# Kernel tuning notes

Hardware: AMD Instinct MI355X
Metric: run time of the kernel (lower is better)

Reference implementation:

```python
import jax, jax.numpy as jnp
import numpy as np

N_NODES = 20000
N_EDGES = 320000
IN_DIM = 256
HIDDEN = 256
OUT_DIM = 128
N_LAYERS = 3
N_GROUPS = 4
EXP_PER_GROUP = 2
N_EXPERTS = N_GROUPS * EXP_PER_GROUP
TOP_K = 2


def setup_inputs() -> dict:
    key = jax.random.key(0)
    ks = jax.random.split(key, 12)
    d = HIDDEN
    r = 2 * d  # router/expert input dim: concat(node, neighbor-mean)
    x = jax.random.normal(ks[0], (N_NODES, IN_DIM), dtype=jnp.float32)
    edge_index = jax.random.randint(ks[1], (2, N_EDGES), 0, N_NODES, dtype=jnp.int32)
    s = 0.05
    Wg = jax.random.normal(ks[2], (N_LAYERS, r, N_GROUPS), dtype=jnp.float32) * s
    We = jax.random.normal(ks[3], (N_LAYERS, r, N_EXPERTS), dtype=jnp.float32) * s
    Ww = jax.random.normal(ks[4], (N_LAYERS, r, d), dtype=jnp.float32) * s
    W1 = jax.random.normal(ks[5], (N_LAYERS, N_EXPERTS, r, d), dtype=jnp.float32) * s
    b1 = jnp.zeros((N_LAYERS, N_EXPERTS, d), dtype=jnp.float32)
    W2 = jax.random.normal(ks[6], (N_LAYERS, N_EXPERTS, d, d), dtype=jnp.float32) * s
    b2 = jnp.zeros((N_LAYERS, N_EXPERTS, d), dtype=jnp.float32)
    wc = jax.random.normal(ks[7], (N_LAYERS, r, 1), dtype=jnp.float32) * s
    Wout = jax.random.normal(ks[8], (d, OUT_DIM), dtype=jnp.float32) * s
    return {"x": x, "edge_index": edge_index, "Wg": Wg, "We": We, "Ww": Ww,
            "W1": W1, "b1": b1, "W2": W2, "b2": b2, "wc": wc, "Wout": Wout}


def _moe_layer(h, src, dst, deg, Wg, We, Ww, W1, b1, W2, b2, wc):
    N = h.shape[0]
    # graph message passing: mean aggregation over incoming edges
    agg = jax.ops.segment_sum(h[src], dst, num_segments=N) / deg  # [N, d]
    r = jnp.concatenate([h, agg], axis=-1)  # [N, 2d] combined router input
    # hierarchical routing: group softmax x within-group expert softmax
    gp = jax.nn.softmax(r @ Wg, axis=-1)                                # [N, G]
    ep = jax.nn.softmax((r @ We).reshape(N, N_GROUPS, EXP_PER_GROUP), axis=-1)
    probs = (gp[..., None] * ep).reshape(N, N_EXPERTS)                  # [N, E]
    # top-k gating, renormalized
    topv, topi = jax.lax.top_k(probs, TOP_K)
    gates = jnp.zeros_like(probs).at[jnp.arange(N)[:, None], topi].set(topv)
    gates = gates / (gates.sum(-1, keepdims=True) + 1e-9)              # [N, E]
    # strong experts: per-expert 2-layer MLP, combined by gates
    hid = jax.nn.relu(jnp.einsum('nf,efd->ned', r, W1) + b1[None])      # [N, E, d]
    exp_out = jnp.einsum('ned,edo->neo', hid, W2) + b2[None]            # [N, E, d]
    strong = jnp.einsum('ne,neo->no', gates, exp_out)                   # [N, d]
    # weak shared expert + confidence gate blend
    weak = r @ Ww                                                       # [N, d]
    conf = jax.nn.sigmoid(r @ wc)                                       # [N, 1]
    return jax.nn.relu(conf * strong + (1.0 - conf) * weak)


def reference(x, edge_index, Wg, We, Ww, W1, b1, W2, b2, wc, Wout):
    src, dst = edge_index[0], edge_index[1]
    N = x.shape[0]
    deg = jax.ops.segment_sum(jnp.ones((edge_index.shape[1],), jnp.float32), dst,
                              num_segments=N)
    deg = jnp.maximum(deg, 1.0)[:, None]
    h = x
    for l in range(Wg.shape[0]):  # small fixed layer loop
        h = _moe_layer(h, src, dst, deg, Wg[l], We[l], Ww[l],
                       W1[l], b1[l], W2[l], b2[l], wc[l])
    return h @ Wout
```

## Files before the change

### kernel.cpp

```cpp
#include <hip/hip_runtime.h>

#define NN 20000
#define NEDGE 320000
#define D 256
#define RD 512
#define OD 128
#define NEXP 8
#define NSLOT (2*NN)
#define NODE_BLOCKS 79
#define ASSIGN_BLOCKS 157

typedef unsigned short u16;
typedef __attribute__((ext_vector_type(8))) short short8v;
typedef __attribute__((ext_vector_type(16))) float f32x16;

__device__ __forceinline__ void split1(float v, u16& h, u16& m, u16& l) {
    unsigned b = __float_as_uint(v);
    h = (u16)(b >> 16);
    float fh = __uint_as_float(b & 0xffff0000u);
    float r1 = v - fh;
    unsigned b1 = __float_as_uint(r1);
    m = (u16)(b1 >> 16);
    float fm = __uint_as_float(b1 & 0xffff0000u);
    float r2 = r1 - fm;
    l = (u16)(__float_as_uint(r2) >> 16);
}

__device__ __forceinline__ void split8(const float4& x, const float4& y,
                                       short8v& h, short8v& m, short8v& l) {
    float v[8] = {x.x, x.y, x.z, x.w, y.x, y.y, y.z, y.w};
#pragma unroll
    for (int i = 0; i < 8; i++) {
        u16 hh, mm, ll;
        split1(v[i], hh, mm, ll);
        h[i] = (short)hh; m[i] = (short)mm; l[i] = (short)ll;
    }
}


__global__ void copy_x_zero_cnt_k(const float* __restrict__ x, float* __restrict__ r,
                                  int* __restrict__ cnt) {
    int gid = blockIdx.x * 256 + threadIdx.x;
    int n = gid >> 6;
    int c4 = gid & 63;
    if (gid < NN * (D / 4)) {
        float4 v = reinterpret_cast<const float4*>(x)[gid];
        reinterpret_cast<float4*>(r + (size_t)n * RD)[c4] = v;
    }
    if (gid < NN) cnt[gid] = 0;
}

__global__ void count_edges_k(const int* __restrict__ dst, int* __restrict__ cnt) {
    int e = blockIdx.x * 256 + threadIdx.x;
    if (e < NEDGE) atomicAdd(&cnt[dst[e]], 1);
}

__global__ void block_sums_k(const int* __restrict__ cnt, int* __restrict__ bsum) {
    __shared__ int s[256];
    int i = blockIdx.x * 256 + threadIdx.x;
    s[threadIdx.x] = (i < NN) ? cnt[i] : 0;
    __syncthreads();
    for (int off = 128; off > 0; off >>= 1) {
        if (threadIdx.x < off) s[threadIdx.x] += s[threadIdx.x + off];
        __syncthreads();
    }
    if (threadIdx.x == 0) bsum[blockIdx.x] = s[0];
}

__global__ void scan_bsums_k(int* __restrict__ bsum, int* __restrict__ row_start) {
    if (blockIdx.x == 0 && threadIdx.x == 0) {
        int acc = 0;
        for (int i = 0; i < NODE_BLOCKS; i++) { int t = bsum[i]; bsum[i] = acc; acc += t; }
        row_start[NN] = acc;
    }
}

__global__ void block_scan_k(const int* __restrict__ cnt, const int* __restrict__ bsum,
                             int* __restrict__ row_start, int* __restrict__ cur) {
    __shared__ int s[256];
    int i = blockIdx.x * 256 + threadIdx.x;
    int v = (i < NN) ? cnt[i] : 0;
    s[threadIdx.x] = v;
    __syncthreads();
    for (int off = 1; off < 256; off <<= 1) {
        int t = (threadIdx.x >= off) ? s[threadIdx.x - off] : 0;
        __syncthreads();
        s[threadIdx.x] += t;
        __syncthreads();
    }
    int excl = s[threadIdx.x] - v + bsum[blockIdx.x];
    if (i < NN) { row_start[i] = excl; cur[i] = excl; }
}

__global__ void fill_csr_k(const int* __restrict__ src, const int* __restrict__ dst,
                           int* __restrict__ cur, int* __restrict__ csr_src) {
    int e = blockIdx.x * 256 + threadIdx.x;
    if (e < NEDGE) {
        int pos = atomicAdd(&cur[dst[e]], 1);
        csr_src[pos] = src[e];
    }
}

__global__ void aggregate_k(float* __restrict__ r, const int* __restrict__ row_start,
                            const int* __restrict__ csr_src, int* __restrict__ ec) {
    if (blockIdx.x == 0 && threadIdx.x < 16) ec[threadIdx.x] = 0;
    int wid = blockIdx.x * 4 + (threadIdx.x >> 6);
    int lane = threadIdx.x & 63;
    if (wid >= NN) return;
    int beg = row_start[wid], end = row_start[wid + 1];
    float ax = 0.f, ay = 0.f, az = 0.f, aw = 0.f;
    for (int j = beg; j < end; j++) {
        int s = csr_src[j];
        float4 v = reinterpret_cast<const float4*>(r + (size_t)s * RD)[lane];
        ax += v.x; ay += v.y; az += v.z; aw += v.w;
    }
    float deg = (float)((end - beg) > 1 ? (end - beg) : 1);
    float4 o = make_float4(ax / deg, ay / deg, az / deg, aw / deg);
    reinterpret_cast<float4*>(r + (size_t)wid * RD + D)[lane] = o;
}

__global__ void router_k(const float* __restrict__ r, const float* __restrict__ Wg,
                         const float* __restrict__ We, const float* __restrict__ wc,
                         int* __restrict__ node_top, float* __restrict__ node_gate,
                         float* __restrict__ conf) {
    int wid = blockIdx.x * 4 + (threadIdx.x >> 6);
    int lane = threadIdx.x & 63;
    if (wid >= NN) return;

    const float* rrow = r + (size_t)wid * RD;
    float pg[4] = {0, 0, 0, 0};
    float pe[8] = {0, 0, 0, 0, 0, 0, 0, 0};
    float pc = 0.f;
#pragma unroll
    for (int i = 0; i < 8; i++) {
        int k = lane + i * 64;
        float rv = rrow[k];
        float4 wg = *reinterpret_cast<const float4*>(Wg + (size_t)k * 4);
        pg[0] = fmaf(rv, wg.x, pg[0]); pg[1] = fmaf(rv, wg.y, pg[1]);
        pg[2] = fmaf(rv, wg.z, pg[2]); pg[3] = fmaf(rv, wg.w, pg[3]);
        float4 w0 = *reinterpret_cast<const float4*>(We + (size_t)k * 8);
        float4 w1 = *reinterpret_cast<const float4*>(We + (size_t)k * 8 + 4);
        pe[0] = fmaf(rv, w0.x, pe[0]); pe[1] = fmaf(rv, w0.y, pe[1]);
        pe[2] = fmaf(rv, w0.z, pe[2]); pe[3] = fmaf(rv, w0.w, pe[3]);
        pe[4] = fmaf(rv, w1.x, pe[4]); pe[5] = fmaf(rv, w1.y, pe[5]);
        pe[6] = fmaf(rv, w1.z, pe[6]); pe[7] = fmaf(rv, w1.w, pe[7]);
        pc = fmaf(rv, wc[k], pc);
    }
#pragma unroll
    for (int off = 32; off > 0; off >>= 1) {
#pragma unroll
        for (int g = 0; g < 4; g++) pg[g] += __shfl_xor(pg[g], off);
#pragma unroll
        for (int g = 0; g < 8; g++) pe[g] += __shfl_xor(pe[g], off);
        pc += __shfl_xor(pc, off);
    }

    if (lane == 0) {
        float m = fmaxf(fmaxf(pg[0], pg[1]), fmaxf(pg[2], pg[3]));
        float eg[4]; float sg = 0.f;
#pragma unroll
        for (int g = 0; g < 4; g++) { eg[g] = expf(pg[g] - m); sg += eg[g]; }
        float probs[8];
#pragma unroll
        for (int g = 0; g < 4; g++) {
            float a = pe[2 * g], b = pe[2 * g + 1];
            float mm = fmaxf(a, b);
            float ea = expf(a - mm), eb = expf(b - mm);
            float inv = 1.f / (ea + eb);
            float gp = eg[g] / sg;
            probs[2 * g]     = gp * ea * inv;
            probs[2 * g + 1] = gp * eb * inv;
        }
        int i0 = 0; float v0 = probs[0];
#pragma unroll
        for (int j = 1; j < 8; j++) if (probs[j] > v0) { v0 = probs[j]; i0 = j; }
        int i1 = -1; float v1 = -1e30f;
#pragma unroll
        for (int j = 0; j < 8; j++) if (j != i0 && probs[j] > v1) { v1 = probs[j]; i1 = j; }
        float s = v0 + v1 + 1e-9f;
        node_top[2 * wid] = i0;  node_top[2 * wid + 1] = i1;
        node_gate[2 * wid] = v0 / s;  node_gate[2 * wid + 1] = v1 / s;
        conf[wid] = 1.f / (1.f + expf(-pc));
    }
}

__global__ void expert_hist_k(const int* __restrict__ node_top, int* __restrict__ ec) {
    __shared__ int h[NEXP];
    if (threadIdx.x < NEXP) h[threadIdx.x] = 0;
    __syncthreads();
    int i = blockIdx.x * 256 + threadIdx.x;
    if (i < NSLOT) atomicAdd(&h[node_top[i]], 1);
    __syncthreads();
    if (threadIdx.x < NEXP && h[threadIdx.x] > 0) atomicAdd(&ec[threadIdx.x], h[threadIdx.x]);
}

__global__ void expert_scan_k(const int* __restrict__ ec, int* __restrict__ es,
                              int* __restrict__ ecur) {
    if (blockIdx.x == 0 && threadIdx.x == 0) {
        int acc = 0;
        for (int e = 0; e < NEXP; e++) { es[e] = acc; acc += ec[e]; ecur[e] = 0; }
        es[NEXP] = acc;
    }
}

__global__ void fill_experts_k(const int* __restrict__ node_top, const float* __restrict__ node_gate,
                               const int* __restrict__ es, int* __restrict__ ecur,
                               int* __restrict__ slot_node, float* __restrict__ slot_gate,
                               int* __restrict__ node_slot) {
    __shared__ int hcnt[NEXP], hbase[NEXP];
    int tid = threadIdx.x;
    if (tid < NEXP) hcnt[tid] = 0;
    __syncthreads();
    int i = blockIdx.x * 256 + tid;
    int e = 0, local = 0;
    bool act = (i < NSLOT);
    if (act) {
        e = node_top[i];
        local = atomicAdd(&hcnt[e], 1);
    }
    __syncthreads();
    if (tid < NEXP) hbase[tid] = (hcnt[tid] > 0) ? atomicAdd(&ecur[tid], hcnt[tid]) : 0;
    __syncthreads();
    if (act) {
        int slot = es[e] + hbase[e] + local;
        slot_node[slot] = i >> 1;
        slot_gate[slot] = node_gate[i];
        node_slot[i] = slot;
    }
}

__global__ void combine_k(const float* __restrict__ expout, const float* __restrict__ weak,
                          const float* __restrict__ conf, const int* __restrict__ node_slot,
                          float* __restrict__ r) {
    int gid = blockIdx.x * 256 + threadIdx.x;
    if (gid >= NN * (D / 4)) return;
    int n = gid >> 6, c4 = gid & 63;
    int s0 = node_slot[2 * n], s1 = node_slot[2 * n + 1];
    float4 e0 = reinterpret_cast<const float4*>(expout + (size_t)s0 * D)[c4];
    float4 e1 = reinterpret_cast<const float4*>(expout + (size_t)s1 * D)[c4];
    float4 w  = reinterpret_cast<const float4*>(weak + (size_t)n * D)[c4];
    float cf = conf[n], cg = 1.f - cf;
    float4 o;
    o.x = fmaxf(cf * (e0.x + e1.x) + cg * w.x, 0.f);
    o.y = fmaxf(cf * (e0.y + e1.y) + cg * w.y, 0.f);
    o.z = fmaxf(cf * (e0.z + e1.z) + cg * w.z, 0.f);
    o.w = fmaxf(cf * (e0.w + e1.w) + cg * w.w, 0.f);
    reinterpret_cast<float4*>(r + (size_t)n * RD)[c4] = o;
}

__global__ void btile_k(const float* __restrict__ src, u16* __restrict__ dH,
                        u16* __restrict__ dM, u16* __restrict__ dL,
                        int K, int N, int total) {
    int gid = blockIdx.x * 256 + threadIdx.x;
    if (gid >= total) return;
    int l = gid & 63;
    int tile = gid >> 6;
    int K16 = K >> 4;
    int kb = tile % K16;
    int t2 = tile / K16;
    int N32 = N >> 5;
    int nb = t2 % N32;
    int mat = t2 / N32;
    int kbase = (kb << 4) + ((l >> 5) << 3);
    int n = (nb << 5) + (l & 31);
    const float* s = src + ((size_t)mat * K + kbase) * N + n;
    short8v vh, vm, vl;
#pragma unroll
    for (int j = 0; j < 8; j++) {
        u16 hh, mm, ll;
        split1(s[(size_t)j * N], hh, mm, ll);
        vh[j] = (short)hh; vm[j] = (short)mm; vl[j] = (short)ll;
    }
    size_t o = (size_t)gid * 8;
    *reinterpret_cast<short8v*>(dH + o) = vh;
    *reinterpret_cast<short8v*>(dM + o) = vm;
    *reinterpret_cast<short8v*>(dL + o) = vl;
}

template <int MODE>
__global__ __launch_bounds__(256, 3) void gemm_mfma(
    const float* __restrict__ A, int lda,
    const u16* __restrict__ BH, const u16* __restrict__ BM,
    const u16* __restrict__ BL,
    const float* __restrict__ bias,
    float* __restrict__ C, int ldc,
    const int* __restrict__ es,
    const int* __restrict__ slot_node,
    const float* __restrict__ slot_gate,
    int M, int N, int K) {
    constexpr int LDK2 = 24;
    constexpr int PL2 = 128 * LDK2;
    __shared__ u16 sA[3 * PL2];

    int tid = threadIdx.x;
    int row0, valid_rows;
    if (MODE == 0) {
        row0 = blockIdx.x * 128;
        valid_rows = M - row0; if (valid_rows > 128) valid_rows = 128;
    } else {
        int bx = blockIdx.x, acc0 = 0, expert = -1, mt = 0;
        row0 = 0; valid_rows = 0;
        for (int e = 0; e < NEXP; e++) {
            int c = es[e + 1] - es[e];
            int t = (c + 127) >> 7;
            if (bx < acc0 + t) {
                expert = e; mt = bx - acc0; row0 = es[e] + (mt << 7);
                valid_rows = c - (mt << 7); if (valid_rows > 128) valid_rows = 128;
                break;
            }
            acc0 += t;
        }
        if (expert < 0) return;
        size_t bo = (size_t)expert * N * K;
        BH += bo; BM += bo; BL += bo;
        bias += expert * D;
    }
    int ncol0 = blockIdx.y * 128;

    int srow = tid >> 1;
    int koff = (tid & 1) * 8;
    int grow;
    {
        int i0 = row0 + srow;
        if (MODE == 1) {
            i0 = i0 < NSLOT ? i0 : NSLOT - 1;
            grow = slot_node[i0];
        } else {
            grow = i0 < M ? i0 : M - 1;
        }
    }
    const float* pA = A + (size_t)grow * lda + koff;

    int lane = tid & 63;
    int wr = ((tid >> 7) & 1) * 64;
    int wc = ((tid >> 6) & 1) * 64;
    int fl = lane & 31;
    int fh8 = (lane >> 5) * 8;
    int K16 = K >> 4;
    int nb0 = (ncol0 + wc) >> 5;
    size_t tb0 = ((size_t)nb0 * K16) * 512 + (size_t)lane * 8;
    size_t tb1 = ((size_t)(nb0 + 1) * K16) * 512 + (size_t)lane * 8;

    f32x16 acc[2][2] = {};
    int aoff = srow * LDK2 + koff;
    const u16* Af0 = sA + (wr + fl) * LDK2 + fh8;
    const u16* Af1 = Af0 + 32 * LDK2;

    for (int kt = 0; kt < K; kt += 16) {
        float4 av0 = *reinterpret_cast<const float4*>(pA + kt);
        float4 av1 = *reinterpret_cast<const float4*>(pA + kt + 4);
        size_t o0 = tb0 + (size_t)(kt >> 4) * 512;
        size_t o1 = tb1 + (size_t)(kt >> 4) * 512;
        short8v bH0 = *reinterpret_cast<const short8v*>(BH + o0);
        short8v bM0 = *reinterpret_cast<const short8v*>(BM + o0);
        short8v bL0 = *reinterpret_cast<const short8v*>(BL + o0);
        short8v bH1 = *reinterpret_cast<const short8v*>(BH + o1);
        short8v bM1 = *reinterpret_cast<const short8v*>(BM + o1);
        short8v bL1 = *reinterpret_cast<const short8v*>(BL + o1);
        __syncthreads();
        {
            short8v h, m, l;
            split8(av0, av1, h, m, l);
            *reinterpret_cast<short8v*>(&sA[0 * PL2 + aoff]) = h;
            *reinterpret_cast<short8v*>(&sA[1 * PL2 + aoff]) = m;
            *reinterpret_cast<short8v*>(&sA[2 * PL2 + aoff]) = l;
        }
        __syncthreads();
        short8v aH0 = *reinterpret_cast<const short8v*>(Af0);
        short8v aM0 = *reinterpret_cast<const short8v*>(Af0 + PL2);
        short8v aL0 = *reinterpret_cast<const short8v*>(Af0 + 2 * PL2);
        short8v aH1 = *reinterpret_cast<const short8v*>(Af1);
        short8v aM1 = *reinterpret_cast<const short8v*>(Af1 + PL2);
        short8v aL1 = *reinterpret_cast<const short8v*>(Af1 + 2 * PL2);
#define MFMA_ACC(d, a, b) d = __builtin_amdgcn_mfma_f32_32x32x16_bf16(a, b, d, 0, 0, 0)
        MFMA_ACC(acc[0][0], aH0, bH0); MFMA_ACC(acc[0][0], aH0, bM0);
        MFMA_ACC(acc[0][0], aM0, bH0); MFMA_ACC(acc[0][0], aH0, bL0);
        MFMA_ACC(acc[0][0], aM0, bM0); MFMA_ACC(acc[0][0], aL0, bH0);
        MFMA_ACC(acc[0][1], aH0, bH1); MFMA_ACC(acc[0][1], aH0, bM1);
        MFMA_ACC(acc[0][1], aM0, bH1); MFMA_ACC(acc[0][1], aH0, bL1);
        MFMA_ACC(acc[0][1], aM0, bM1); MFMA_ACC(acc[0][1], aL0, bH1);
        MFMA_ACC(acc[1][0], aH1, bH0); MFMA_ACC(acc[1][0], aH1, bM0);
        MFMA_ACC(acc[1][0], aM1, bH0); MFMA_ACC(acc[1][0], aH1, bL0);
        MFMA_ACC(acc[1][0], aM1, bM0); MFMA_ACC(acc[1][0], aL1, bH0);
        MFMA_ACC(acc[1][1], aH1, bH1); MFMA_ACC(acc[1][1], aH1, bM1);
        MFMA_ACC(acc[1][1], aM1, bH1); MFMA_ACC(acc[1][1], aH1, bL1);
        MFMA_ACC(acc[1][1], aM1, bM1); MFMA_ACC(acc[1][1], aL1, bH1);
#undef MFMA_ACC
    }

    int fh = lane >> 5;
#pragma unroll
    for (int i = 0; i < 2; i++) {
#pragma unroll
        for (int j = 0; j < 2; j++) {
            int colg = ncol0 + wc + j * 32 + fl;
            float bv = (MODE != 0) ? bias[colg] : 0.f;
#pragma unroll
            for (int rg = 0; rg < 16; rg++) {
                int lrow = wr + i * 32 + (rg & 3) + 8 * (rg >> 2) + 4 * fh;
                if (lrow >= valid_rows) continue;
                int growo = row0 + lrow;
                float v = acc[i][j][rg] + bv;
                if (MODE == 1) {
                    v = fmaxf(v, 0.f);
                } else if (MODE == 2) {
                    v *= slot_gate[growo];
                }
                C[(size_t)growo * ldc + colg] = v;
            }
        }
    }
}

extern "C" void kernel_launch(void* const* d_in, const int* in_sizes, int n_in,
                              void* d_out, int out_size, void* d_ws, size_t ws_size,
                              hipStream_t stream) {
    (void)in_sizes; (void)n_in; (void)out_size; (void)ws_size;
    const float* x    = (const float*)d_in[0];
    const int*   ei   = (const int*)d_in[1];
    const float* Wg   = (const float*)d_in[2];
    const float* We   = (const float*)d_in[3];
    const float* Ww   = (const float*)d_in[4];
    const float* W1   = (const float*)d_in[5];
    const float* b1   = (const float*)d_in[6];
    const float* W2   = (const float*)d_in[7];
    const float* b2   = (const float*)d_in[8];
    const float* wcp  = (const float*)d_in[9];
    const float* Wout = (const float*)d_in[10];
    float* out = (float*)d_out;

    char* p = (char*)d_ws;
    auto alloc = [&](size_t bytes) -> char* {
        char* q = p; p += (bytes + 255) & ~(size_t)255; return q;
    };
    int*   cnt       = (int*)alloc((size_t)NN * 4);
    int*   row_start = (int*)alloc((size_t)(NN + 1) * 4);
    int*   cur       = (int*)alloc((size_t)NN * 4);
    int*   bsum      = (int*)alloc(128 * 4);
    int*   csr_src   = (int*)alloc((size_t)NEDGE * 4);
    float* r         = (float*)alloc((size_t)NN * RD * 4);
    float* hid       = (float*)alloc((size_t)NSLOT * D * 4);
    float* expout    = (float*)alloc((size_t)NSLOT * D * 4);
    float* conf      = (float*)alloc((size_t)NN * 4);
    int*   node_top  = (int*)alloc((size_t)2 * NN * 4);
    float* node_gate = (float*)alloc((size_t)2 * NN * 4);
    int*   node_slot = (int*)alloc((size_t)2 * NN * 4);
    int*   slot_node = (int*)alloc((size_t)NSLOT * 4);
    float* slot_gate = (float*)alloc((size_t)NSLOT * 4);
    int*   ec        = (int*)alloc(64 * 4);
    int*   es        = (int*)alloc(64 * 4);
    int*   ecur      = (int*)alloc(64 * 4);
    u16* w1tH = (u16*)alloc((size_t)NEXP * D * RD * 2);
    u16* w1tM = (u16*)alloc((size_t)NEXP * D * RD * 2);
    u16* w1tL = (u16*)alloc((size_t)NEXP * D * RD * 2);
    u16* w2tH = (u16*)alloc((size_t)NEXP * D * D * 2);
    u16* w2tM = (u16*)alloc((size_t)NEXP * D * D * 2);
    u16* w2tL = (u16*)alloc((size_t)NEXP * D * D * 2);
    u16* wwtH = (u16*)alloc((size_t)D * RD * 2);
    u16* wwtM = (u16*)alloc((size_t)D * RD * 2);
    u16* wwtL = (u16*)alloc((size_t)D * RD * 2);
    u16* wotH = (u16*)alloc((size_t)OD * D * 2);
    u16* wotM = (u16*)alloc((size_t)OD * D * 2);
    u16* wotL = (u16*)alloc((size_t)OD * D * 2);
    float* weak = hid;

    const int* srcp = ei;
    const int* dstp = ei + NEDGE;
    const int EB = (NEDGE + 255) / 256;

    copy_x_zero_cnt_k<<<5000, 256, 0, stream>>>(x, r, cnt);
    count_edges_k<<<EB, 256, 0, stream>>>(dstp, cnt);
    block_sums_k<<<NODE_BLOCKS, 256, 0, stream>>>(cnt, bsum);
    scan_bsums_k<<<1, 64, 0, stream>>>(bsum, row_start);
    block_scan_k<<<NODE_BLOCKS, 256, 0, stream>>>(cnt, bsum, row_start, cur);
    fill_csr_k<<<EB, 256, 0, stream>>>(srcp, dstp, cur, csr_src);
    btile_k<<<16, 256, 0, stream>>>(Wout, wotH, wotM, wotL, D, OD, 4096);

    for (int l = 0; l < 3; l++) {
        btile_k<<<512, 256, 0, stream>>>(W1 + (size_t)l * NEXP * RD * D,
                                         w1tH, w1tM, w1tL, RD, D, 131072);
        btile_k<<<256, 256, 0, stream>>>(W2 + (size_t)l * NEXP * D * D,
                                         w2tH, w2tM, w2tL, D, D, 65536);
        btile_k<<<64, 256, 0, stream>>>(Ww + (size_t)l * RD * D,
                                        wwtH, wwtM, wwtL, RD, D, 16384);
        aggregate_k<<<5000, 256, 0, stream>>>(r, row_start, csr_src, ec);
        router_k<<<5000, 256, 0, stream>>>(r,
            Wg + (size_t)l * RD * 4, We + (size_t)l * RD * 8, wcp + (size_t)l * RD,
            node_top, node_gate, conf);
        expert_hist_k<<<ASSIGN_BLOCKS, 256, 0, stream>>>(node_top, ec);
        expert_scan_k<<<1, 64, 0, stream>>>(ec, es, ecur);
        fill_experts_k<<<ASSIGN_BLOCKS, 256, 0, stream>>>(node_top, node_gate, es, ecur,
                                                          slot_node, slot_gate, node_slot);
        gemm_mfma<1><<<dim3(320, 2), 256, 0, stream>>>(r, RD, w1tH, w1tM, w1tL,
            b1 + (size_t)l * NEXP * D, hid, D, es, slot_node, slot_gate, NSLOT, D, RD);
        gemm_mfma<2><<<dim3(320, 2), 256, 0, stream>>>(hid, D, w2tH, w2tM, w2tL,
            b2 + (size_t)l * NEXP * D, expout, D, es, slot_node, slot_gate, NSLOT, D, D);
        gemm_mfma<0><<<dim3(157, 2), 256, 0, stream>>>(r, RD, wwtH, wwtM, wwtL,
            nullptr, weak, D, nullptr, nullptr, nullptr, NN, D, RD);
        combine_k<<<5000, 256, 0, stream>>>(expout, weak, conf, node_slot, r);
    }
    gemm_mfma<0><<<dim3(157, 1), 256, 0, stream>>>(r, RD, wotH, wotM, wotL,
        nullptr, out, OD, nullptr, nullptr, nullptr, NN, OD, D);
}
```

Before: 840.8 us.

## Double-buffer A tile in LDS and prefetch next K-slice in GEMM

Reworks the MFMA GEMM main loop to ping-pong between two LDS buffers holding the split bf16 A tile. The next K-slice's global loads are issued before computing the current one, which halves the barriers per 16-wide K step and overlaps load latency with MFMA work. In exchange LDS use doubles and launch bounds drop from 3 to 2 blocks per CU, which can lower occupancy and latency hiding. It also assumes K is a multiple of 32.

Measured after the change: 873.7 us. 1.04x slower.

```diff
diff --git a/kernel.cpp b/kernel.cpp
--- a/kernel.cpp
+++ b/kernel.cpp
@@ -278,7 +278,7 @@
 }
 
 template <int MODE>
-__global__ __launch_bounds__(256, 3) void gemm_mfma(
+__global__ __launch_bounds__(256, 2) void gemm_mfma(
     const float* __restrict__ A, int lda,
     const u16* __restrict__ BH, const u16* __restrict__ BM,
     const u16* __restrict__ BL,
@@ -290,7 +290,7 @@
     int M, int N, int K) {
     constexpr int LDK2 = 24;
     constexpr int PL2 = 128 * LDK2;
-    __shared__ u16 sA[3 * PL2];
+    __shared__ u16 sA[6 * PL2];
 
     int tid = threadIdx.x;
     int row0, valid_rows;
@@ -343,35 +343,24 @@
 
     f32x16 acc[2][2] = {};
     int aoff = srow * LDK2 + koff;
-    const u16* Af0 = sA + (wr + fl) * LDK2 + fh8;
-    const u16* Af1 = Af0 + 32 * LDK2;
-
-    for (int kt = 0; kt < K; kt += 16) {
-        float4 av0 = *reinterpret_cast<const float4*>(pA + kt);
-        float4 av1 = *reinterpret_cast<const float4*>(pA + kt + 4);
-        size_t o0 = tb0 + (size_t)(kt >> 4) * 512;
-        size_t o1 = tb1 + (size_t)(kt >> 4) * 512;
-        short8v bH0 = *reinterpret_cast<const short8v*>(BH + o0);
-        short8v bM0 = *reinterpret_cast<const short8v*>(BM + o0);
-        short8v bL0 = *reinterpret_cast<const short8v*>(BL + o0);
-        short8v bH1 = *reinterpret_cast<const short8v*>(BH + o1);
-        short8v bM1 = *reinterpret_cast<const short8v*>(BM + o1);
-        short8v bL1 = *reinterpret_cast<const short8v*>(BL + o1);
-        __syncthreads();
-        {
-            short8v h, m, l;
-            split8(av0, av1, h, m, l);
-            *reinterpret_cast<short8v*>(&sA[0 * PL2 + aoff]) = h;
-            *reinterpret_cast<short8v*>(&sA[1 * PL2 + aoff]) = m;
-            *reinterpret_cast<short8v*>(&sA[2 * PL2 + aoff]) = l;
-        }
-        __syncthreads();
-        short8v aH0 = *reinterpret_cast<const short8v*>(Af0);
-        short8v aM0 = *reinterpret_cast<const short8v*>(Af0 + PL2);
-        short8v aL0 = *reinterpret_cast<const short8v*>(Af0 + 2 * PL2);
-        short8v aH1 = *reinterpret_cast<const short8v*>(Af1);
-        short8v aM1 = *reinterpret_cast<const short8v*>(Af1 + PL2);
-        short8v aL1 = *reinterpret_cast<const short8v*>(Af1 + 2 * PL2);
+
+    auto stage = [&](u16* buf, const float4& x, const float4& y) {
+        short8v h, m, l;
+        split8(x, y, h, m, l);
+        *reinterpret_cast<short8v*>(buf + 0 * PL2 + aoff) = h;
+        *reinterpret_cast<short8v*>(buf + 1 * PL2 + aoff) = m;
+        *reinterpret_cast<short8v*>(buf + 2 * PL2 + aoff) = l;
+    };
+    auto do_tile = [&](const u16* buf, short8v bH0, short8v bM0, short8v bL0,
+                       short8v bH1, short8v bM1, short8v bL1) {
+        const u16* A0 = buf + (wr + fl) * LDK2 + fh8;
+        const u16* A1 = A0 + 32 * LDK2;
+        short8v aH0 = *reinterpret_cast<const short8v*>(A0);
+        short8v aM0 = *reinterpret_cast<const short8v*>(A0 + PL2);
+        short8v aL0 = *reinterpret_cast<const short8v*>(A0 + 2 * PL2);
+        short8v aH1 = *reinterpret_cast<const short8v*>(A1);
+        short8v aM1 = *reinterpret_cast<const short8v*>(A1 + PL2);
+        short8v aL1 = *reinterpret_cast<const short8v*>(A1 + 2 * PL2);
 #define MFMA_ACC(d, a, b) d = __builtin_amdgcn_mfma_f32_32x32x16_bf16(a, b, d, 0, 0, 0)
         MFMA_ACC(acc[0][0], aH0, bH0); MFMA_ACC(acc[0][0], aH0, bM0);
         MFMA_ACC(acc[0][0], aM0, bH0); MFMA_ACC(acc[0][0], aH0, bL0);
@@ -386,6 +375,51 @@
         MFMA_ACC(acc[1][1], aM1, bH1); MFMA_ACC(acc[1][1], aH1, bL1);
         MFMA_ACC(acc[1][1], aM1, bM1); MFMA_ACC(acc[1][1], aL1, bH1);
 #undef MFMA_ACC
+    };
+
+    float4 av0 = *reinterpret_cast<const float4*>(pA);
+    float4 av1 = *reinterpret_cast<const float4*>(pA + 4);
+    short8v cH0 = *reinterpret_cast<const short8v*>(BH + tb0);
+    short8v cM0 = *reinterpret_cast<const short8v*>(BM + tb0);
+    short8v cL0 = *reinterpret_cast<const short8v*>(BL + tb0);
+    short8v cH1 = *reinterpret_cast<const short8v*>(BH + tb1);
+    short8v cM1 = *reinterpret_cast<const short8v*>(BM + tb1);
+    short8v cL1 = *reinterpret_cast<const short8v*>(BL + tb1);
+    stage(sA, av0, av1);
+    __syncthreads();
+
+    for (int kt = 0; kt < K; kt += 32) {
+        float4 nv0 = *reinterpret_cast<const float4*>(pA + kt + 16);
+        float4 nv1 = *reinterpret_cast<const float4*>(pA + kt + 20);
+        size_t o0 = tb0 + (size_t)((kt >> 4) + 1) * 512;
+        size_t o1 = tb1 + (size_t)((kt >> 4) + 1) * 512;
+        short8v nH0 = *reinterpret_cast<const short8v*>(BH + o0);
+        short8v nM0 = *reinterpret_cast<const short8v*>(BM + o0);
+        short8v nL0 = *reinterpret_cast<const short8v*>(BL + o0);
+        short8v nH1 = *reinterpret_cast<const short8v*>(BH + o1);
+        short8v nM1 = *reinterpret_cast<const short8v*>(BM + o1);
+        short8v nL1 = *reinterpret_cast<const short8v*>(BL + o1);
+        do_tile(sA, cH0, cM0, cL0, cH1, cM1, cL1);
+        stage(sA + 3 * PL2, nv0, nv1);
+        __syncthreads();
+        bool more = (kt + 32 < K);
+        if (more) {
+            av0 = *reinterpret_cast<const float4*>(pA + kt + 32);
+            av1 = *reinterpret_cast<const float4*>(pA + kt + 36);
+            o0 = tb0 + (size_t)((kt >> 4) + 2) * 512;
+            o1 = tb1 + (size_t)((kt >> 4) + 2) * 512;
+            cH0 = *reinterpret_cast<const short8v*>(BH + o0);
+            cM0 = *reinterpret_cast<const short8v*>(BM + o0);
+            cL0 = *reinterpret_cast<const short8v*>(BL + o0);
+            cH1 = *reinterpret_cast<const short8v*>(BH + o1);
+            cM1 = *reinterpret_cast<const short8v*>(BM + o1);
+            cL1 = *reinterpret_cast<const short8v*>(BL + o1);
+        }
+        do_tile(sA + 3 * PL2, nH0, nM0, nL0, nH1, nM1, nL1);
+        if (more) {
+            stage(sA, av0, av1);
+        }
+        __syncthreads();
     }
 
     int fh = lane >> 5;
```

## Halve GEMM row tile to 64 with swizzled fragment LDS layout

Applied to the files above, without the earlier changes.

The 3-way bf16-split MFMA GEMM's row tile shrinks from 128 to 64. Each wave now computes 32x64 instead of 64x64, and the grids double, so more blocks are resident and the tail is smaller. The A tile is stored in LDS in an MFMA-fragment-ordered layout without padding, and launch bounds rise to 5 blocks/CU. The cost is that each B fragment is reused across half as many rows, which roughly doubles B-tile global traffic per output and lowers MFMA work per barrier.

Measured after the change: 825.3 us. Within noise of the previous version (-1.9%).

```diff
diff --git a/kernel.cpp b/kernel.cpp
--- a/kernel.cpp
+++ b/kernel.cpp
@@ -11,6 +11,7 @@
 #define ASSIGN_BLOCKS 157
 
 typedef unsigned short u16;
+typedef __attribute__((ext_vector_type(4))) short short4v;
 typedef __attribute__((ext_vector_type(8))) short short8v;
 typedef __attribute__((ext_vector_type(16))) float f32x16;
 
@@ -24,17 +25,6 @@
     float fm = __uint_as_float(b1 & 0xffff0000u);
     float r2 = r1 - fm;
     l = (u16)(__float_as_uint(r2) >> 16);
-}
-
-__device__ __forceinline__ void split8(const float4& x, const float4& y,
-                                       short8v& h, short8v& m, short8v& l) {
-    float v[8] = {x.x, x.y, x.z, x.w, y.x, y.y, y.z, y.w};
-#pragma unroll
-    for (int i = 0; i < 8; i++) {
-        u16 hh, mm, ll;
-        split1(v[i], hh, mm, ll);
-        h[i] = (short)hh; m[i] = (short)mm; l[i] = (short)ll;
-    }
 }
 
 
@@ -278,7 +268,7 @@
 }
 
 template <int MODE>
-__global__ __launch_bounds__(256, 3) void gemm_mfma(
+__global__ __launch_bounds__(256, 5) void gemm_mfma(
     const float* __restrict__ A, int lda,
     const u16* __restrict__ BH, const u16* __restrict__ BM,
     const u16* __restrict__ BL,
@@ -288,37 +278,36 @@
     const int* __restrict__ slot_node,
     const float* __restrict__ slot_gate,
     int M, int N, int K) {
-    constexpr int LDK2 = 24;
-    constexpr int PL2 = 128 * LDK2;
+    constexpr int PL2 = 1024;
     __shared__ u16 sA[3 * PL2];
 
     int tid = threadIdx.x;
     int row0, valid_rows;
     if (MODE == 0) {
-        row0 = blockIdx.x * 128;
-        valid_rows = M - row0; if (valid_rows > 128) valid_rows = 128;
+        row0 = blockIdx.x * 64;
+        valid_rows = M - row0; if (valid_rows > 64) valid_rows = 64;
     } else {
         int bx = blockIdx.x, acc0 = 0, expert = -1, mt = 0;
         row0 = 0; valid_rows = 0;
         for (int e = 0; e < NEXP; e++) {
             int c = es[e + 1] - es[e];
-            int t = (c + 127) >> 7;
+            int t = (c + 63) >> 6;
             if (bx < acc0 + t) {
-                expert = e; mt = bx - acc0; row0 = es[e] + (mt << 7);
-                valid_rows = c - (mt << 7); if (valid_rows > 128) valid_rows = 128;
+                expert = e; mt = bx - acc0; row0 = es[e] + (mt << 6);
+                valid_rows = c - (mt << 6); if (valid_rows > 64) valid_rows = 64;
                 break;
             }
             acc0 += t;
         }
         if (expert < 0) return;
-        size_t bo = (size_t)expert * N * K;
+        int bo = expert * N * K;
         BH += bo; BM += bo; BL += bo;
         bias += expert * D;
     }
     int ncol0 = blockIdx.y * 128;
 
-    int srow = tid >> 1;
-    int koff = (tid & 1) * 8;
+    int srow = tid >> 2;
+    int koff = (tid & 3) * 4;
     int grow;
     {
         int i0 = row0 + srow;
@@ -330,84 +319,77 @@
         }
     }
     const float* pA = A + (size_t)grow * lda + koff;
+    int woff = ((srow >> 5) * 2 + (koff >> 3)) * 256 + (srow & 31) * 8 + (koff & 4);
 
     int lane = tid & 63;
-    int wr = ((tid >> 7) & 1) * 64;
-    int wc = ((tid >> 6) & 1) * 64;
+    int wave = tid >> 6;
+    int wr = (wave & 1) * 32;
+    int wc = (wave >> 1) * 64;
     int fl = lane & 31;
-    int fh8 = (lane >> 5) * 8;
     int K16 = K >> 4;
     int nb0 = (ncol0 + wc) >> 5;
-    size_t tb0 = ((size_t)nb0 * K16) * 512 + (size_t)lane * 8;
-    size_t tb1 = ((size_t)(nb0 + 1) * K16) * 512 + (size_t)lane * 8;
-
-    f32x16 acc[2][2] = {};
-    int aoff = srow * LDK2 + koff;
-    const u16* Af0 = sA + (wr + fl) * LDK2 + fh8;
-    const u16* Af1 = Af0 + 32 * LDK2;
+    int tbase0 = nb0 * K16 * 512 + lane * 8;
+    int tbase1 = (nb0 + 1) * K16 * 512 + lane * 8;
+    int roff = ((wr >> 5) * 2 + (lane >> 5)) * 256 + fl * 8;
+
+    f32x16 acc0 = {};
+    f32x16 acc1 = {};
 
     for (int kt = 0; kt < K; kt += 16) {
-        float4 av0 = *reinterpret_cast<const float4*>(pA + kt);
-        float4 av1 = *reinterpret_cast<const float4*>(pA + kt + 4);
-        size_t o0 = tb0 + (size_t)(kt >> 4) * 512;
-        size_t o1 = tb1 + (size_t)(kt >> 4) * 512;
-        short8v bH0 = *reinterpret_cast<const short8v*>(BH + o0);
-        short8v bM0 = *reinterpret_cast<const short8v*>(BM + o0);
-        short8v bL0 = *reinterpret_cast<const short8v*>(BL + o0);
-        short8v bH1 = *reinterpret_cast<const short8v*>(BH + o1);
-        short8v bM1 = *reinterpret_cast<const short8v*>(BM + o1);
-        short8v bL1 = *reinterpret_cast<const short8v*>(BL + o1);
+        float4 av = *reinterpret_cast<const float4*>(pA + kt);
+        int ko = (kt >> 4) * 512;
+        short8v bH0 = *reinterpret_cast<const short8v*>(BH + tbase0 + ko);
+        short8v bM0 = *reinterpret_cast<const short8v*>(BM + tbase0 + ko);
+        short8v bL0 = *reinterpret_cast<const short8v*>(BL + tbase0 + ko);
+        short8v bH1 = *reinterpret_cast<const short8v*>(BH + tbase1 + ko);
+        short8v bM1 = *reinterpret_cast<const short8v*>(BM + tbase1 + ko);
+        short8v bL1 = *reinterpret_cast<const short8v*>(BL + tbase1 + ko);
         __syncthreads();
         {
-            short8v h, m, l;
-            split8(av0, av1, h, m, l);
-            *reinterpret_cast<short8v*>(&sA[0 * PL2 + aoff]) = h;
-            *reinterpret_cast<short8v*>(&sA[1 * PL2 + aoff]) = m;
-            *reinterpret_cast<short8v*>(&sA[2 * PL2 + aoff]) = l;
+            u16 h0, m0, l0, h1, m1, l1, h2, m2, l2, h3, m3, l3;
+            split1(av.x, h0, m0, l0);
+            split1(av.y, h1, m1, l1);
+            split1(av.z, h2, m2, l2);
+            split1(av.w, h3, m3, l3);
+            short4v hv = {(short)h0, (short)h1, (short)h2, (short)h3};
+            short4v mv = {(short)m0, (short)m1, (short)m2, (short)m3};
+            short4v lv = {(short)l0, (short)l1, (short)l2, (short)l3};
+            *reinterpret_cast<short4v*>(&sA[0 * PL2 + woff]) = hv;
+            *reinterpret_cast<short4v*>(&sA[1 * PL2 + woff]) = mv;
+            *reinterpret_cast<short4v*>(&sA[2 * PL2 + woff]) = lv;
         }
         __syncthreads();
-        short8v aH0 = *reinterpret_cast<const short8v*>(Af0);
-        short8v aM0 = *reinterpret_cast<const short8v*>(Af0 + PL2);
-        short8v aL0 = *reinterpret_cast<const short8v*>(Af0 + 2 * PL2);
-        short8v aH1 = *reinterpret_cast<const short8v*>(Af1);
-        short8v aM1 = *reinterpret_cast<const short8v*>(Af1 + PL2);
-        short8v aL1 = *reinterpret_cast<const short8v*>(Af1 + 2 * PL2);
+        short8v aH = *reinterpret_cast<const short8v*>(&sA[0 * PL2 + roff]);
+        short8v aM = *reinterpret_cast<const short8v*>(&sA[1 * PL2 + roff]);
+        short8v aL = *reinterpret_cast<const short8v*>(&sA[2 * PL2 + roff]);
 #define MFMA_ACC(d, a, b) d = __builtin_amdgcn_mfma_f32_32x32x16_bf16(a, b, d, 0, 0, 0)
-        MFMA_ACC(acc[0][0], aH0, bH0); MFMA_ACC(acc[0][0], aH0, bM0);
-        MFMA_ACC(acc[0][0], aM0, bH0); MFMA_ACC(acc[0][0], aH0, bL0);
-        MFMA_ACC(acc[0][0], aM0, bM0); MFMA_ACC(acc[0][0], aL0, bH0);
-        MFMA_ACC(acc[0][1], aH0, bH1); MFMA_ACC(acc[0][1], aH0, bM1);
-        MFMA_ACC(acc[0][1], aM0, bH1); MFMA_ACC(acc[0][1], aH0, bL1);
-        MFMA_ACC(acc[0][1], aM0, bM1); MFMA_ACC(acc[0][1], aL0, bH1);
-        MFMA_ACC(acc[1][0], aH1, bH0); MFMA_ACC(acc[1][0], aH1, bM0);
-        MFMA_ACC(acc[1][0], aM1, bH0); MFMA_ACC(acc[1][0], aH1, bL0);
-        MFMA_ACC(acc[1][0], aM1, bM0); MFMA_ACC(acc[1][0], aL1, bH0);
-        MFMA_ACC(acc[1][1], aH1, bH1); MFMA_ACC(acc[1][1], aH1, bM1);
-        MFMA_ACC(acc[1][1], aM1, bH1); MFMA_ACC(acc[1][1], aH1, bL1);
-        MFMA_ACC(acc[1][1], aM1, bM1); MFMA_ACC(acc[1][1], aL1, bH1);
+        MFMA_ACC(acc0, aH, bH0); MFMA_ACC(acc0, aH, bM0);
+        MFMA_ACC(acc0, aM, bH0); MFMA_ACC(acc0, aH, bL0);
+        MFMA_ACC(acc0, aM, bM0); MFMA_ACC(acc0, aL, bH0);
+        MFMA_ACC(acc1, aH, bH1); MFMA_ACC(acc1, aH, bM1);
+        MFMA_ACC(acc1, aM, bH1); MFMA_ACC(acc1, aH, bL1);
+        MFMA_ACC(acc1, aM, bM1); MFMA_ACC(acc1, aL, bH1);
 #undef MFMA_ACC
     }
 
     int fh = lane >> 5;
 #pragma unroll
-    for (int i = 0; i < 2; i++) {
-#pragma unroll
-        for (int j = 0; j < 2; j++) {
-            int colg = ncol0 + wc + j * 32 + fl;
-            float bv = (MODE != 0) ? bias[colg] : 0.f;
-#pragma unroll
-            for (int rg = 0; rg < 16; rg++) {
-                int lrow = wr + i * 32 + (rg & 3) + 8 * (rg >> 2) + 4 * fh;
-                if (lrow >= valid_rows) continue;
-                int growo = row0 + lrow;
-                float v = acc[i][j][rg] + bv;
-                if (MODE == 1) {
-                    v = fmaxf(v, 0.f);
-                } else if (MODE == 2) {
-                    v *= slot_gate[growo];
-                }
-                C[(size_t)growo * ldc + colg] = v;
+    for (int j = 0; j < 2; j++) {
+        const f32x16& a = j ? acc1 : acc0;
+        int colg = ncol0 + wc + j * 32 + fl;
+        float bv = (MODE != 0) ? bias[colg] : 0.f;
+#pragma unroll
+        for (int rg = 0; rg < 16; rg++) {
+            int lrow = wr + (rg & 3) + 8 * (rg >> 2) + 4 * fh;
+            if (lrow >= valid_rows) continue;
+            int growo = row0 + lrow;
+            float v = a[rg] + bv;
+            if (MODE == 1) {
+                v = fmaxf(v, 0.f);
+            } else if (MODE == 2) {
+                v *= slot_gate[growo];
             }
+            C[(size_t)growo * ldc + colg] = v;
         }
     }
 }
@@ -491,14 +473,14 @@
         expert_scan_k<<<1, 64, 0, stream>>>(ec, es, ecur);
         fill_experts_k<<<ASSIGN_BLOCKS, 256, 0, stream>>>(node_top, node_gate, es, ecur,
                                                           slot_node, slot_gate, node_slot);
-        gemm_mfma<1><<<dim3(320, 2), 256, 0, stream>>>(r, RD, w1tH, w1tM, w1tL,
+        gemm_mfma<1><<<dim3(640, 2), 256, 0, stream>>>(r, RD, w1tH, w1tM, w1tL,
             b1 + (size_t)l * NEXP * D, hid, D, es, slot_node, slot_gate, NSLOT, D, RD);
-        gemm_mfma<2><<<dim3(320, 2), 256, 0, stream>>>(hid, D, w2tH, w2tM, w2tL,
+        gemm_mfma<2><<<dim3(640, 2), 256, 0, stream>>>(hid, D, w2tH, w2tM, w2tL,
             b2 + (size_t)l * NEXP * D, expout, D, es, slot_node, slot_gate, NSLOT, D, D);
-        gemm_mfma<0><<<dim3(157, 2), 256, 0, stream>>>(r, RD, wwtH, wwtM, wwtL,
+        gemm_mfma<0><<<dim3(313, 2), 256, 0, stream>>>(r, RD, wwtH, wwtM, wwtL,
             nullptr, weak, D, nullptr, nullptr, nullptr, NN, D, RD);
         combine_k<<<5000, 256, 0, stream>>>(expout, weak, conf, node_slot, r);
     }
-    gemm_mfma<0><<<dim3(157, 1), 256, 0, stream>>>(r, RD, wotH, wotM, wotL,
+    gemm_mfma<0><<<dim3(313, 1), 256, 0, stream>>>(r, RD, wotH, wotM, wotL,
         nullptr, out, OD, nullptr, nullptr, nullptr, NN, OD, D);
 }
```
